# Performance work log

Hardware: AMD Instinct MI355X
Metric: run time of the kernel (lower is better)

Reference implementation:

```python
import jax, jax.numpy as jnp
import numpy as np

B, V, K = 4, 16384, 16
E, F, D, H, L, ITERS = 32, 2, 64, 4, 2, 10
NEG = -1e9


def setup_inputs() -> dict:
    key = jax.random.key(0)
    ks = jax.random.split(key, 24)
    def g(k, shape, fan_in):
        return jax.random.normal(k, shape, dtype=jnp.float32) * (fan_in ** -0.5)
    inp = {}
    inp["node_embeddings"] = jax.random.normal(ks[0], (B, V, E), dtype=jnp.float32)
    inp["node_features"] = jax.random.normal(ks[1], (B, V, F), dtype=jnp.float32)
    inp["demands"] = jax.random.normal(ks[2], (B, V, 1), dtype=jnp.float32)
    # padded adjacency list; value == V means masked (no neighbor)
    inp["adj_lst"] = jax.random.randint(ks[3], (B, V, K), 0, V + 1, dtype=jnp.int32)
    # precomputed inverse-adjacency indices; reference computes inflow by scatter-add instead
    inp["flow_indices"] = jax.random.randint(ks[4], (B, V, K), 0, V, dtype=jnp.int32)
    inp["num_nodes"] = V
    din = E + F
    inp["W_enc1"] = g(ks[5], (din, D), din); inp["b_enc1"] = jnp.zeros((D,), jnp.float32)
    inp["W_enc2"] = g(ks[6], (D, D), D); inp["b_enc2"] = jnp.zeros((D,), jnp.float32)
    inp["W_gat"] = g(ks[7], (H, D, D), D)
    inp["a_src"] = g(ks[8], (H, D), D)
    inp["a_dst"] = g(ks[9], (H, D), D)
    for i, nm in enumerate(["z", "r", "c"]):
        inp["W_" + nm] = g(ks[10 + 2 * i], (D, D), D)
        inp["U_" + nm] = g(ks[11 + 2 * i], (D, D), D)
        inp["b_" + nm] = jnp.zeros((D,), jnp.float32)
    inp["W_dec1"] = g(ks[16], (D, D), D); inp["b_dec1"] = jnp.zeros((D,), jnp.float32)
    inp["W_dec2"] = g(ks[17], (D, 1), D); inp["b_dec2"] = jnp.zeros((1,), jnp.float32)
    return inp


def _forward(node_embeddings, node_features, demands,
             W_enc1, b_enc1, W_enc2, b_enc2,
             W_gat, a_src, a_dst,
             W_z, U_z, b_z, W_r, U_r, b_r, W_c, U_c, b_c,
             W_dec1, b_dec1, W_dec2, b_dec2,
             adj_lst, num_nodes):
    Vn = num_nodes
    bidx = jnp.arange(adj_lst.shape[0])[:, None, None]  # [B,1,1]
    mask = adj_lst == Vn  # [B,V,K] padded slots

    # --- node encoder MLP (tanh, activate_final=True) ---
    x = jnp.concatenate([node_embeddings, node_features], axis=-1)
    h = jnp.tanh(x @ W_enc1 + b_enc1)
    h = jnp.tanh(h @ W_enc2 + b_enc2)

    def gather_nodes(t):
        # masked_gather: pad with a zero row so index == num_nodes reads zeros
        t_pad = jnp.concatenate([t, jnp.zeros_like(t[:, :1])], axis=1)  # [B,V+1,Dt]
        return t_pad[bidx, adj_lst]  # [B,V,K,Dt]

    # --- graph_layers x (AdjGAT + GRU) ---
    for _ in range(L):
        agg = 0.0
        for hd in range(H):
            t = h @ W_gat[hd]                       # [B,V,D]
            nb = gather_nodes(t)                    # [B,V,K,D]
            scores = (t @ a_src[hd])[:, :, None] + nb @ a_dst[hd]  # [B,V,K]
            attn = jax.nn.softmax(jnp.where(mask, NEG, scores), axis=-1)
            agg = agg + jnp.einsum('bvk,bvkd->bvd', attn, nb)
        m = jnp.tanh(agg / H)
        z = jax.nn.sigmoid(m @ W_z + h @ U_z + b_z)
        r = jax.nn.sigmoid(m @ W_r + h @ U_r + b_r)
        c = jnp.tanh(m @ W_c + (r * h) @ U_c + b_c)
        h = (1.0 - z) * h + z * c

    # --- decoder -> per-edge weights via masked gather + softmax ---
    node_w = jnp.tanh(h @ W_dec1 + b_dec1) @ W_dec2 + b_dec2   # [B,V,1]
    pw = gather_nodes(node_w)[..., 0]                          # [B,V,K]
    norm_w = jax.nn.softmax(jnp.where(mask, NEG, pw), axis=-1)

    # --- iterative min-cost-flow solver ---
    flow0 = norm_w * jax.nn.relu(-demands)  # sources (demand<0) push supply
    def body(carry, _):
        flow, _ = carry
        inflow = jnp.zeros((flow.shape[0], Vn + 1), flow.dtype)
        inflow = inflow.at[bidx, adj_lst].add(flow)[:, :Vn]    # [B,V]
        new = norm_w * jax.nn.relu(inflow[..., None] - demands)
        return (new, flow), None
    (flow, pflow), _ = jax.lax.scan(body, (flow0, flow0), None, length=ITERS)

    flow_cost = jnp.sum(flow * flow, axis=(1, 2))  # quadratic cost_fn
    return flow, flow_cost, norm_w, pflow


def reference(node_embeddings, node_features, demands, adj_lst, flow_indices, num_nodes,
              W_enc1, b_enc1, W_enc2, b_enc2, W_gat, a_src, a_dst,
              W_z, U_z, b_z, W_r, U_r, b_r, W_c, U_c, b_c,
              W_dec1, b_dec1, W_dec2, b_dec2):
    # flow_indices is the precomputed inverse adjacency; inflow is computed
    # equivalently here by scatter-add over adj_lst.
    return _forward(node_embeddings, node_features, demands,
                    W_enc1, b_enc1, W_enc2, b_enc2,
                    W_gat, a_src, a_dst,
                    W_z, U_z, b_z, W_r, U_r, b_r, W_c, U_c, b_c,
                    W_dec1, b_dec1, W_dec2, b_dec2,
                    adj_lst, num_nodes)
```

## Files before the change

### kernel.cpp

```cpp
#include <hip/hip_runtime.h>
#include <stdint.h>
#include <math.h>

#define BN 4
#define VN 16384
#define KN 16
#define HN 4
#define NN (BN*VN)
#define EN (VN*KN)
#define CAP 64
#define NEGC (-1.0e9f)

typedef __attribute__((ext_vector_type(8))) short short8;
typedef __attribute__((ext_vector_type(4))) float floatx4;
typedef __attribute__((ext_vector_type(2))) float floatx2;
typedef unsigned short u16;
typedef unsigned int u32;

#define OFF_H      0ull
#define OFF_M      8388608ull
#define OFF_T      16777216ull
#define OFF_SSRC   50331648ull
#define OFF_SDST   51380224ull
#define OFF_NW     52428800ull
#define OFF_NV     52690944ull
#define OFF_CNT    53215232ull
#define OFF_PG     53477376ull
#define OFF_PZR    (OFF_PG  + 32768ull)
#define OFF_PC     (OFF_PZR + 32768ull)
#define OFF_PE1    (OFF_PC  + 16384ull)
#define OFF_PE2    (OFF_PE1 + 8192ull)
#define OFF_PD1    (OFF_PE2 + 8192ull)

__device__ __forceinline__ u16 f2bf(float x){
  union { float f; unsigned int u; } c; c.f = x;
  unsigned int r = c.u + 0x7fffu + ((c.u >> 16) & 1u);
  return (u16)(r >> 16);
}
__device__ __forceinline__ float bf2f(u32 s){
  union { unsigned int u; float f; } c; c.u = s << 16;
  return c.f;
}
__device__ __forceinline__ float sigm(float x){ return 1.0f/(1.0f+expf(-x)); }

union S8 { short8 v; u16 u[8]; };

__global__ __launch_bounds__(256) void k_pack(
    const float* __restrict__ Wg,  const float* __restrict__ Wz, const float* __restrict__ Uz,
    const float* __restrict__ Wr,  const float* __restrict__ Ur, const float* __restrict__ Wc,
    const float* __restrict__ Uc,  const float* __restrict__ We1, const float* __restrict__ We2,
    const float* __restrict__ Wd1,
    u16* __restrict__ pg, u16* __restrict__ pzr, u16* __restrict__ pc,
    u16* __restrict__ pe1, u16* __restrict__ pe2, u16* __restrict__ pd1)
{
  int e = blockIdx.x*256 + threadIdx.x;
  int el; u16* dst; int CN; int region;
  if      (e < 16384){ el = e;        dst = pg;  CN = 2; region = 0; }
  else if (e < 32768){ el = e-16384;  dst = pzr; CN = 4; region = 1; }
  else if (e < 40960){ el = e-32768;  dst = pc;  CN = 4; region = 2; }
  else if (e < 45056){ el = e-40960;  dst = pe1; CN = 2; region = 3; }
  else if (e < 49152){ el = e-45056;  dst = pe2; CN = 2; region = 4; }
  else               { el = e-49152;  dst = pd1; CN = 2; region = 5; }
  int j    = el & 7;
  int lane = (el >> 3) & 63;
  int rest = el >> 9;
  int c  = rest % CN;
  int ng = rest / CN;
  int k  = c*32 + (lane>>4)*8 + j;
  int n  = ng*16 + (lane&15);
  float val = 0.0f;
  if (region == 0){
    val = Wg[(size_t)(n>>6)*4096 + k*64 + (n&63)];
  } else if (region == 1){
    int km = (k&3)*16 + ((k>>2)&15);
    if (n < 64) val = (k<64) ? Wz[km*64+n]      : Uz[(k-64)*64+n];
    else        val = (k<64) ? Wr[km*64+(n-64)] : Ur[(k-64)*64+(n-64)];
  } else if (region == 2){
    int km = (k&3)*16 + ((k>>2)&15);
    val = (k<64) ? Wc[km*64+n] : Uc[(k-64)*64+n];
  } else if (region == 3){
    val = (k<34) ? We1[k*64+n] : 0.0f;
  } else if (region == 4){
    val = We2[k*64+n];
  } else {
    val = Wd1[k*64+n];
  }
  dst[el] = f2bf(val);
}

template<int CN>
__device__ __forceinline__ void load_b(const u16* p, int chunk, int lane, short8 Bf[CN][4]){
  const short8* P = (const short8*)p;
  #pragma unroll
  for (int c=0;c<CN;c++)
    #pragma unroll
    for (int ng=0; ng<4; ng++)
      Bf[c][ng] = P[((chunk*4+ng)*CN + c)*64 + lane];
}

template<int CN>
__device__ __forceinline__ void mfma_tile(const short8* A, const short8 Bf[CN][4],
                                          floatx4 acc[4][4], int wave, int lane){
  #pragma unroll
  for (int c=0;c<CN;c++){
    #pragma unroll
    for (int mg=0;mg<4;mg++){
      short8 a = A[((wave*4+mg)*CN + c)*64 + lane];
      #pragma unroll
      for (int ng=0;ng<4;ng++)
        acc[mg][ng] = __builtin_amdgcn_mfma_f32_16x16x32_bf16(a, Bf[c][ng], acc[mg][ng], 0, 0, 0);
    }
  }
}

__device__ __forceinline__ void zero_acc(floatx4 acc[4][4]){
  #pragma unroll
  for (int mg=0;mg<4;mg++)
    #pragma unroll
    for (int ng=0;ng<4;ng++){
      floatx4 z = {0.f,0.f,0.f,0.f};
      acc[mg][ng] = z;
    }
}

__global__ __launch_bounds__(128) void k_enc(
    const float* __restrict__ emb, const float* __restrict__ feat,
    const u16* __restrict__ pe1, const u16* __restrict__ pe2,
    const float* __restrict__ be1, const float* __restrict__ be2,
    u16* __restrict__ hout, u32* __restrict__ cnt)
{
  cnt[blockIdx.x*128 + threadIdx.x] = 0u;
  __shared__ short8 A1[1024];
  __shared__ short8 A2[1024];
  const int tid = threadIdx.x;
  const int n0  = blockIdx.x * 128;
  for (int it=0; it<8; ++it){
    int slot = it*128 + tid;
    int row = slot >> 3, jc = slot & 7;
    S8 w;
    if (jc < 4){
      const float* s = emb + (size_t)(n0+row)*32 + jc*8;
      #pragma unroll
      for (int j=0;j<8;j++) w.u[j] = f2bf(s[j]);
    } else if (jc == 4){
      const float* s = feat + (size_t)(n0+row)*2;
      w.u[0] = f2bf(s[0]); w.u[1] = f2bf(s[1]);
      #pragma unroll
      for (int j=2;j<8;j++) w.u[j] = 0;
    } else {
      #pragma unroll
      for (int j=0;j<8;j++) w.u[j] = 0;
    }
    A1[((row>>4)*2 + (jc>>2))*64 + (jc&3)*16 + (row&15)] = w.v;
  }
  __syncthreads();
  const int wave = tid>>6, lane = tid&63, q = lane>>4, ml = lane&15;

  short8 Bf[2][4];
  load_b<2>(pe1, 0, lane, Bf);
  floatx4 acc[4][4];
  zero_acc(acc);
  mfma_tile<2>(A1, Bf, acc, wave, lane);

  u16* A2s = (u16*)A2;
  #pragma unroll
  for (int mg=0;mg<4;mg++){
    #pragma unroll
    for (int r=0;r<4;r++){
      int row_l = wave*64 + mg*16 + q*4 + r;
      #pragma unroll
      for (int ng=0;ng<4;ng++){
        int k2 = ng*16 + ml;
        float v = tanhf(acc[mg][ng][r] + be1[k2]);
        int c2 = k2>>5, q2=(k2>>3)&3, j2=k2&7;
        A2s[ (((row_l>>4)*2 + c2)*64 + q2*16 + (row_l&15))*8 + j2 ] = f2bf(v);
      }
    }
  }
  __syncthreads();

  load_b<2>(pe2, 0, lane, Bf);
  zero_acc(acc);
  mfma_tile<2>(A2, Bf, acc, wave, lane);
  #pragma unroll
  for (int mg=0;mg<4;mg++)
    #pragma unroll
    for (int r=0;r<4;r++){
      int row = n0 + wave*64 + mg*16 + q*4 + r;
      #pragma unroll
      for (int ng=0;ng<4;ng++){
        int col = ng*16 + ml;
        hout[(size_t)row*64 + col] = f2bf(tanhf(acc[mg][ng][r] + be2[col]));
      }
    }
}

__global__ __launch_bounds__(128) void k_t(
    const u16* __restrict__ h, const u16* __restrict__ pg,
    const float* __restrict__ asrc, const float* __restrict__ adst,
    u32* __restrict__ tq, float* __restrict__ ssrc, float* __restrict__ sdst)
{
  __shared__ short8 A[1024];
  const int tid = threadIdx.x;
  const int n0  = blockIdx.x * 128;
  const short8* hp = (const short8*)h;
  for (int it=0; it<8; ++it){
    int slot = it*128 + tid;
    int row = slot >> 3, jc = slot & 7;
    A[((row>>4)*2 + (jc>>2))*64 + (jc&3)*16 + (row&15)] = hp[(size_t)(n0+row)*8 + jc];
  }
  __syncthreads();
  const int wave = tid>>6, lane = tid&63, q = lane>>4, ml = lane&15;

  for (int chunk=0; chunk<4; ++chunk){
    short8 Bf[2][4];
    load_b<2>(pg, chunk, lane, Bf);
    floatx4 acc[4][4];
    zero_acc(acc);
    mfma_tile<2>(A, Bf, acc, wave, lane);

    float as[4], ad[4];
    #pragma unroll
    for (int ng=0;ng<4;ng++){
      as[ng] = asrc[chunk*64 + ng*16 + ml];
      ad[ng] = adst[chunk*64 + ng*16 + ml];
    }
    #pragma unroll
    for (int mg=0;mg<4;mg++){
      #pragma unroll
      for (int r=0;r<4;r++){
        int row = n0 + wave*64 + mg*16 + q*4 + r;
        float v0 = acc[mg][0][r], v1 = acc[mg][1][r];
        float v2 = acc[mg][2][r], v3 = acc[mg][3][r];
        int pk = __builtin_amdgcn_cvt_pk_fp8_f32(v0, v1, 0, false);
        pk     = __builtin_amdgcn_cvt_pk_fp8_f32(v2, v3, pk, true);
        tq[(size_t)row*64 + chunk*16 + ml] = (u32)pk;
        float ps = v0*as[0] + v1*as[1] + v2*as[2] + v3*as[3];
        float pd = v0*ad[0] + v1*ad[1] + v2*ad[2] + v3*ad[3];
        #pragma unroll
        for (int s=1;s<16;s<<=1){ ps += __shfl_xor(ps, s, 64); pd += __shfl_xor(pd, s, 64); }
        if (ml == 0){ ssrc[row*4 + chunk] = ps; sdst[row*4 + chunk] = pd; }
      }
    }
  }
}

__global__ __launch_bounds__(256) void k_attn(
    const int* __restrict__ adj, const u32* __restrict__ tq,
    const float* __restrict__ ssrc, const float* __restrict__ sdst,
    u16* __restrict__ m)
{
  const int wave = threadIdx.x>>6, lane = threadIdx.x&63;
  const int nid = blockIdx.x*4 + wave;
  const int b = nid >> 14;
  const int hd = lane>>4;
  int u = adj[(size_t)nid*16 + (lane&15)];
  float sc = (u == VN) ? NEGC : (ssrc[nid*4 + hd] + sdst[((size_t)b*VN + u)*4 + hd]);
  float mx = sc;
  #pragma unroll
  for (int s=1;s<16;s<<=1) mx = fmaxf(mx, __shfl_xor(mx, s, 64));
  float ex = expf(sc - mx);
  float sm = ex;
  #pragma unroll
  for (int s=1;s<16;s<<=1) sm += __shfl_xor(sm, s, 64);
  float attn = ex / sm;

  float a0=0.f, a1=0.f, a2=0.f, a3=0.f;
  const int srcl = lane & 48;
  #pragma unroll
  for (int k2=0;k2<16;k2++){
    int u2 = __shfl(u, k2, 64);
    float av = __shfl(attn, srcl + k2, 64);
    u32 w = tq[((size_t)b*VN + u2)*64 + lane];
    floatx2 f01 = __builtin_amdgcn_cvt_pk_f32_fp8((int)w, false);
    floatx2 f23 = __builtin_amdgcn_cvt_pk_f32_fp8((int)w, true);
    a0 += av*f01.x; a1 += av*f01.y; a2 += av*f23.x; a3 += av*f23.y;
  }
  a0 += __shfl_xor(a0,16,64); a0 += __shfl_xor(a0,32,64);
  a1 += __shfl_xor(a1,16,64); a1 += __shfl_xor(a1,32,64);
  a2 += __shfl_xor(a2,16,64); a2 += __shfl_xor(a2,32,64);
  a3 += __shfl_xor(a3,16,64); a3 += __shfl_xor(a3,32,64);
  if (lane < 16){
    union { uint2 v; u16 u[4]; } val;
    val.u[0] = f2bf(tanhf(a0*0.25f)); val.u[1] = f2bf(tanhf(a1*0.25f));
    val.u[2] = f2bf(tanhf(a2*0.25f)); val.u[3] = f2bf(tanhf(a3*0.25f));
    *(uint2*)(m + (size_t)nid*64 + lane*4) = val.v;
  }
}

__global__ __launch_bounds__(128) void k_gru(
    const u16* __restrict__ m, u16* __restrict__ h,
    const u16* __restrict__ pzr, const u16* __restrict__ pc_,
    const float* __restrict__ bz, const float* __restrict__ br,
    const float* __restrict__ bc_)
{
  __shared__ short8 A[2048];
  const int tid = threadIdx.x;
  const int n0  = blockIdx.x * 128;
  const short8* mp = (const short8*)m;
  const short8* hp = (const short8*)h;
  for (int it=0; it<16; ++it){
    int slot = it*128 + tid;
    int row = slot >> 4, jc = slot & 15;
    short8 w = (jc < 8) ? mp[(size_t)(n0+row)*8 + jc]
                        : hp[(size_t)(n0+row)*8 + (jc-8)];
    A[((row>>4)*4 + (jc>>2))*64 + (jc&3)*16 + (row&15)] = w;
  }
  __syncthreads();
  const int wave = tid>>6, lane = tid&63, q = lane>>4, ml = lane&15;

  short8 Bf[4][4];

  floatx4 zacc[4][4];
  load_b<4>(pzr, 0, lane, Bf);
  zero_acc(zacc);
  mfma_tile<4>(A, Bf, zacc, wave, lane);

  floatx4 acc[4][4];
  load_b<4>(pzr, 1, lane, Bf);
  zero_acc(acc);
  mfma_tile<4>(A, Bf, acc, wave, lane);

  floatx4 h_old[4][4];
  u16* As = (u16*)A;
  #pragma unroll
  for (int mg=0;mg<4;mg++){
    #pragma unroll
    for (int r=0;r<4;r++){
      int row_l = wave*64 + mg*16 + q*4 + r;
      int row   = n0 + row_l;
      #pragma unroll
      for (int ng=0;ng<4;ng++){
        int col = ng*16 + ml;
        float rv = sigm(acc[mg][ng][r] + br[col]);
        float hv = bf2f(h[(size_t)row*64 + col]);
        h_old[mg][ng][r] = hv;
        int kk = 64 + col;
        int c2 = kk>>5, q2 = (kk>>3)&3, j2 = kk&7;
        As[ (((row_l>>4)*4 + c2)*64 + q2*16 + (row_l&15))*8 + j2 ] = f2bf(hv*rv);
      }
    }
  }

  load_b<4>(pc_, 0, lane, Bf);
  zero_acc(acc);
  mfma_tile<4>(A, Bf, acc, wave, lane);

  #pragma unroll
  for (int mg=0;mg<4;mg++)
    #pragma unroll
    for (int r=0;r<4;r++){
      int row = n0 + wave*64 + mg*16 + q*4 + r;
      #pragma unroll
      for (int ng=0;ng<4;ng++){
        int col = ng*16 + ml;
        float zv = sigm(zacc[mg][ng][r] + bz[col]);
        float cv = tanhf(acc[mg][ng][r] + bc_[col]);
        float ho = h_old[mg][ng][r];
        h[(size_t)row*64 + col] = f2bf((1.f - zv)*ho + zv*cv);
      }
    }
}

__global__ __launch_bounds__(128) void k_dec(
    const u16* __restrict__ h, const u16* __restrict__ pd1,
    const float* __restrict__ bd1, const float* __restrict__ Wd2, const float* __restrict__ bd2,
    float* __restrict__ nodew, float* __restrict__ cost)
{
  {
    int t = blockIdx.x*128 + threadIdx.x;
    if (t < BN) cost[t] = 0.f;
  }
  __shared__ short8 A[1024];
  const int tid = threadIdx.x;
  const int n0  = blockIdx.x * 128;
  const short8* hp = (const short8*)h;
  for (int it=0; it<8; ++it){
    int slot = it*128 + tid;
    int row = slot >> 3, jc = slot & 7;
    A[((row>>4)*2 + (jc>>2))*64 + (jc&3)*16 + (row&15)] = hp[(size_t)(n0+row)*8 + jc];
  }
  __syncthreads();
  const int wave = tid>>6, lane = tid&63, q = lane>>4, ml = lane&15;

  short8 Bf[2][4];
  load_b<2>(pd1, 0, lane, Bf);
  floatx4 acc[4][4];
  zero_acc(acc);
  mfma_tile<2>(A, Bf, acc, wave, lane);

  float wd2l[4];
  #pragma unroll
  for (int ng=0;ng<4;ng++) wd2l[ng] = Wd2[ng*16 + ml];
  float b2 = bd2[0];
  #pragma unroll
  for (int mg=0;mg<4;mg++)
    #pragma unroll
    for (int r=0;r<4;r++){
      int row = n0 + wave*64 + mg*16 + q*4 + r;
      float ps = 0.f;
      #pragma unroll
      for (int ng=0;ng<4;ng++)
        ps += tanhf(acc[mg][ng][r] + bd1[ng*16+ml]) * wd2l[ng];
      #pragma unroll
      for (int s=1;s<16;s<<=1) ps += __shfl_xor(ps, s, 64);
      if (ml == 0) nodew[row] = ps + b2;
    }
}

__global__ __launch_bounds__(256) void k_pw(
    const int* __restrict__ adj, const float* __restrict__ nodew, const float* __restrict__ dem,
    float* __restrict__ normw, float* __restrict__ nv0,
    u32* __restrict__ cnt, u32* __restrict__ bucket)
{
  int e = blockIdx.x*256 + threadIdx.x;
  int node = e >> 4;
  int b = node >> 14;
  int u = adj[e];
  float pw = (u == VN) ? NEGC : nodew[(size_t)b*VN + u];
  float mx = pw;
  #pragma unroll
  for (int s=1;s<16;s<<=1) mx = fmaxf(mx, __shfl_xor(mx, s, 64));
  float ex = expf(pw - mx);
  float sm = ex;
  #pragma unroll
  for (int s=1;s<16;s<<=1) sm += __shfl_xor(sm, s, 64);
  float nw = ex / sm;
  normw[e] = nw;
  if ((e & 15) == 0) nv0[node] = fmaxf(-dem[node], 0.f);
  if (u < VN){
    int g = b*VN + u;
    u32 pos = atomicAdd(&cnt[g], 1u);
    if (pos < CAP)
      bucket[(size_t)g*CAP + pos] = ((u32)f2bf(nw) << 16) | (u32)(node & (VN-1));
  }
}

__global__ __launch_bounds__(256) void k_gather(
    const u32* __restrict__ cnt, const u32* __restrict__ bucket,
    const float* __restrict__ dem, const float* __restrict__ nvin, float* __restrict__ nvout)
{
  int tid = blockIdx.x*256 + threadIdx.x;
  int g = tid >> 4;
  int lane = tid & 15;
  int b = g >> 14;
  u32 n = cnt[g];
  if (n > CAP) n = CAP;
  const u32* bk = bucket + (size_t)g*CAP;
  const float* nb = nvin + (size_t)b*VN;
  float sum = 0.f;
  for (u32 i = (u32)lane; i < n; i += 16u){
    u32 r = bk[i];
    sum += bf2f(r >> 16) * nb[r & 0xFFFFu];
  }
  #pragma unroll
  for (int sh=1; sh<16; sh<<=1) sum += __shfl_xor(sum, sh, 64);
  if (lane == 0) nvout[g] = fmaxf(sum - dem[g], 0.f);
}

__global__ __launch_bounds__(256) void k_flows(
    const float* __restrict__ normw, const float* __restrict__ nv9,
    const float* __restrict__ nv10,
    float* __restrict__ pflow, float* __restrict__ flow, float* __restrict__ cost)
{
  int e = blockIdx.x*256 + threadIdx.x;
  int node = e >> 4;
  float w = normw[e];
  pflow[e] = w * nv9[node];
  float fl = w * nv10[node];
  flow[e] = fl;
  float ss = fl*fl;
  #pragma unroll
  for (int sh=1; sh<64; sh<<=1) ss += __shfl_xor(ss, sh, 64);
  __shared__ float part[4];
  if ((threadIdx.x & 63) == 0) part[threadIdx.x>>6] = ss;
  __syncthreads();
  if (threadIdx.x == 0) atomicAdd(cost + (e>>18), part[0]+part[1]+part[2]+part[3]);
}

extern "C" void kernel_launch(void* const* d_in, const int* in_sizes, int n_in,
                              void* d_out, int out_size, void* d_ws, size_t ws_size,
                              hipStream_t stream)
{
  const float* emb  = (const float*)d_in[0];
  const float* feat = (const float*)d_in[1];
  const float* dem  = (const float*)d_in[2];
  const int*   adj  = (const int*)  d_in[3];
  const float* We1 = (const float*)d_in[6];
  const float* be1 = (const float*)d_in[7];
  const float* We2 = (const float*)d_in[8];
  const float* be2 = (const float*)d_in[9];
  const float* Wg  = (const float*)d_in[10];
  const float* asrc= (const float*)d_in[11];
  const float* adst= (const float*)d_in[12];
  const float* Wz  = (const float*)d_in[13];
  const float* Uz  = (const float*)d_in[14];
  const float* bz  = (const float*)d_in[15];
  const float* Wr  = (const float*)d_in[16];
  const float* Ur  = (const float*)d_in[17];
  const float* br  = (const float*)d_in[18];
  const float* Wc  = (const float*)d_in[19];
  const float* Uc  = (const float*)d_in[20];
  const float* bc  = (const float*)d_in[21];
  const float* Wd1 = (const float*)d_in[22];
  const float* bd1 = (const float*)d_in[23];
  const float* Wd2 = (const float*)d_in[24];
  const float* bd2 = (const float*)d_in[25];

  char* ws = (char*)d_ws;
  u16*   h     = (u16*)  (ws + OFF_H);
  u16*   m     = (u16*)  (ws + OFF_M);
  u32*   tq    = (u32*)  (ws + OFF_T);
  u32*   bucket= (u32*)  (ws + OFF_T);
  float* ssrc  = (float*)(ws + OFF_SSRC);
  float* sdst  = (float*)(ws + OFF_SDST);
  float* nodew = (float*)(ws + OFF_NW);
  float* nv    = (float*)(ws + OFF_NV);
  u32*   cnt   = (u32*)  (ws + OFF_CNT);
  u16* pg  = (u16*)(ws + OFF_PG);
  u16* pzr = (u16*)(ws + OFF_PZR);
  u16* pc  = (u16*)(ws + OFF_PC);
  u16* pe1 = (u16*)(ws + OFF_PE1);
  u16* pe2 = (u16*)(ws + OFF_PE2);
  u16* pd1 = (u16*)(ws + OFF_PD1);
  float* nv0b = nv;
  float* nv1b = nv + NN;

  float* out0 = (float*)d_out;
  float* out1 = out0 + 1048576;
  float* out2 = out0 + 1048580;
  float* out3 = out0 + 2097156;

  k_pack<<<208, 256, 0, stream>>>(Wg, Wz, Uz, Wr, Ur, Wc, Uc, We1, We2, Wd1,
                                  pg, pzr, pc, pe1, pe2, pd1);
  k_enc<<<512, 128, 0, stream>>>(emb, feat, pe1, pe2, be1, be2, h, cnt);

  for (int l=0; l<2; ++l){
    k_t   <<<512, 128, 0, stream>>>(h, pg, asrc, adst, tq, ssrc, sdst);
    k_attn<<<16384, 256, 0, stream>>>(adj, tq, ssrc, sdst, m);
    k_gru <<<512, 128, 0, stream>>>(m, h, pzr, pc, bz, br, bc);
  }

  k_dec<<<512, 128, 0, stream>>>(h, pd1, bd1, Wd2, bd2, nodew, out1);
  k_pw <<<4096, 256, 0, stream>>>(adj, nodew, dem, out2, nv0b, cnt, bucket);

  for (int i=1; i<=10; ++i){
    float* in  = (i & 1) ? nv0b : nv1b;
    float* out = (i & 1) ? nv1b : nv0b;
    k_gather<<<4096, 256, 0, stream>>>(cnt, bucket, dem, in, out);
  }
  k_flows<<<4096, 256, 0, stream>>>(out2, nv1b, nv0b, out3, out0, out1);
}
```

Baseline: 481.3 us.

## Fold attention vectors into weights and build inverse adjacency with shared atomics

Precomputes W_gat·a_src and W_gat·a_dst per head during packing, so k_t gets the attention scores from one extra small MFMA on the bf16 hidden state. This replaces the per-row dot products and cross-lane shuffle reductions, and the src/dst scores are stored interleaved in one array. The scatter of edges into per-node buckets moves from global atomics in k_pw to a new k_build kernel. Each of its 64 blocks scans the full adjacency of one batch and counts only its 1024 targets with shared-memory atomics. This trades global atomic contention for 16x redundant reads of the adjacency and an extra launch, and computes the scores from bf16 inputs, which slightly changes precision.

```diff
diff --git a/kernel.cpp b/kernel.cpp
--- a/kernel.cpp
+++ b/kernel.cpp
@@ -20,8 +20,7 @@
 #define OFF_H      0ull
 #define OFF_M      8388608ull
 #define OFF_T      16777216ull
-#define OFF_SSRC   50331648ull
-#define OFF_SDST   51380224ull
+#define OFF_SS     50331648ull
 #define OFF_NW     52428800ull
 #define OFF_NV     52690944ull
 #define OFF_CNT    53215232ull
@@ -31,6 +30,7 @@
 #define OFF_PE1    (OFF_PC  + 16384ull)
 #define OFF_PE2    (OFF_PE1 + 8192ull)
 #define OFF_PD1    (OFF_PE2 + 8192ull)
+#define OFF_PAV    (OFF_PD1 + 8192ull)
 
 __device__ __forceinline__ u16 f2bf(float x){
   union { float f; unsigned int u; } c; c.f = x;
@@ -49,18 +49,21 @@
     const float* __restrict__ Wg,  const float* __restrict__ Wz, const float* __restrict__ Uz,
     const float* __restrict__ Wr,  const float* __restrict__ Ur, const float* __restrict__ Wc,
     const float* __restrict__ Uc,  const float* __restrict__ We1, const float* __restrict__ We2,
-    const float* __restrict__ Wd1,
+    const float* __restrict__ Wd1, const float* __restrict__ asrc, const float* __restrict__ adst,
     u16* __restrict__ pg, u16* __restrict__ pzr, u16* __restrict__ pc,
-    u16* __restrict__ pe1, u16* __restrict__ pe2, u16* __restrict__ pd1)
+    u16* __restrict__ pe1, u16* __restrict__ pe2, u16* __restrict__ pd1,
+    u16* __restrict__ pav)
 {
   int e = blockIdx.x*256 + threadIdx.x;
+  if (e >= 54272) return;
   int el; u16* dst; int CN; int region;
   if      (e < 16384){ el = e;        dst = pg;  CN = 2; region = 0; }
   else if (e < 32768){ el = e-16384;  dst = pzr; CN = 4; region = 1; }
   else if (e < 40960){ el = e-32768;  dst = pc;  CN = 4; region = 2; }
   else if (e < 45056){ el = e-40960;  dst = pe1; CN = 2; region = 3; }
   else if (e < 49152){ el = e-45056;  dst = pe2; CN = 2; region = 4; }
-  else               { el = e-49152;  dst = pd1; CN = 2; region = 5; }
+  else if (e < 53248){ el = e-49152;  dst = pd1; CN = 2; region = 5; }
+  else               { el = e-53248;  dst = pav; CN = 2; region = 6; }
   int j    = el & 7;
   int lane = (el >> 3) & 63;
   int rest = el >> 9;
@@ -82,8 +85,16 @@
     val = (k<34) ? We1[k*64+n] : 0.0f;
   } else if (region == 4){
     val = We2[k*64+n];
+  } else if (region == 5){
+    val = Wd1[k*64+n];
   } else {
-    val = Wd1[k*64+n];
+    int hd = (n>>1)&3, s = n&1;
+    const float* av = s ? (adst + hd*64) : (asrc + hd*64);
+    const float* wrow = Wg + (size_t)hd*4096 + k*64;
+    float acc = 0.f;
+    #pragma unroll 8
+    for (int d=0; d<64; d++) acc += wrow[d]*av[d];
+    val = acc;
   }
   dst[el] = f2bf(val);
 }
@@ -127,9 +138,8 @@
     const float* __restrict__ emb, const float* __restrict__ feat,
     const u16* __restrict__ pe1, const u16* __restrict__ pe2,
     const float* __restrict__ be1, const float* __restrict__ be2,
-    u16* __restrict__ hout, u32* __restrict__ cnt)
-{
-  cnt[blockIdx.x*128 + threadIdx.x] = 0u;
+    u16* __restrict__ hout)
+{
   __shared__ short8 A1[1024];
   __shared__ short8 A2[1024];
   const int tid = threadIdx.x;
@@ -196,9 +206,8 @@
 }
 
 __global__ __launch_bounds__(128) void k_t(
-    const u16* __restrict__ h, const u16* __restrict__ pg,
-    const float* __restrict__ asrc, const float* __restrict__ adst,
-    u32* __restrict__ tq, float* __restrict__ ssrc, float* __restrict__ sdst)
+    const u16* __restrict__ h, const u16* __restrict__ pg, const u16* __restrict__ pav,
+    u32* __restrict__ tq, float* __restrict__ ss)
 {
   __shared__ short8 A[1024];
   const int tid = threadIdx.x;
@@ -219,27 +228,32 @@
     zero_acc(acc);
     mfma_tile<2>(A, Bf, acc, wave, lane);
 
-    float as[4], ad[4];
-    #pragma unroll
-    for (int ng=0;ng<4;ng++){
-      as[ng] = asrc[chunk*64 + ng*16 + ml];
-      ad[ng] = adst[chunk*64 + ng*16 + ml];
-    }
     #pragma unroll
     for (int mg=0;mg<4;mg++){
       #pragma unroll
       for (int r=0;r<4;r++){
         int row = n0 + wave*64 + mg*16 + q*4 + r;
-        float v0 = acc[mg][0][r], v1 = acc[mg][1][r];
-        float v2 = acc[mg][2][r], v3 = acc[mg][3][r];
-        int pk = __builtin_amdgcn_cvt_pk_fp8_f32(v0, v1, 0, false);
-        pk     = __builtin_amdgcn_cvt_pk_fp8_f32(v2, v3, pk, true);
+        int pk = __builtin_amdgcn_cvt_pk_fp8_f32(acc[mg][0][r], acc[mg][1][r], 0, false);
+        pk     = __builtin_amdgcn_cvt_pk_fp8_f32(acc[mg][2][r], acc[mg][3][r], pk, true);
         tq[(size_t)row*64 + chunk*16 + ml] = (u32)pk;
-        float ps = v0*as[0] + v1*as[1] + v2*as[2] + v3*as[3];
-        float pd = v0*ad[0] + v1*ad[1] + v2*ad[2] + v3*ad[3];
-        #pragma unroll
-        for (int s=1;s<16;s<<=1){ ps += __shfl_xor(ps, s, 64); pd += __shfl_xor(pd, s, 64); }
-        if (ml == 0){ ssrc[row*4 + chunk] = ps; sdst[row*4 + chunk] = pd; }
+      }
+    }
+  }
+
+  const short8* Pv = (const short8*)pav;
+  short8 Bs0 = Pv[lane], Bs1 = Pv[64 + lane];
+  #pragma unroll
+  for (int mg=0;mg<4;mg++){
+    floatx4 sacc = {0.f,0.f,0.f,0.f};
+    short8 a0 = A[((wave*4+mg)*2 + 0)*64 + lane];
+    short8 a1 = A[((wave*4+mg)*2 + 1)*64 + lane];
+    sacc = __builtin_amdgcn_mfma_f32_16x16x32_bf16(a0, Bs0, sacc, 0, 0, 0);
+    sacc = __builtin_amdgcn_mfma_f32_16x16x32_bf16(a1, Bs1, sacc, 0, 0, 0);
+    if (ml < 8){
+      #pragma unroll
+      for (int r=0;r<4;r++){
+        int row = n0 + wave*64 + mg*16 + q*4 + r;
+        ss[(size_t)row*8 + ml] = sacc[r];
       }
     }
   }
@@ -247,15 +261,14 @@
 
 __global__ __launch_bounds__(256) void k_attn(
     const int* __restrict__ adj, const u32* __restrict__ tq,
-    const float* __restrict__ ssrc, const float* __restrict__ sdst,
-    u16* __restrict__ m)
+    const float* __restrict__ ss, u16* __restrict__ m)
 {
   const int wave = threadIdx.x>>6, lane = threadIdx.x&63;
   const int nid = blockIdx.x*4 + wave;
   const int b = nid >> 14;
   const int hd = lane>>4;
   int u = adj[(size_t)nid*16 + (lane&15)];
-  float sc = (u == VN) ? NEGC : (ssrc[nid*4 + hd] + sdst[((size_t)b*VN + u)*4 + hd]);
+  float sc = (u == VN) ? NEGC : (ss[(size_t)nid*8 + hd*2] + ss[((size_t)b*VN + u)*8 + hd*2 + 1]);
   float mx = sc;
   #pragma unroll
   for (int s=1;s<16;s<<=1) mx = fmaxf(mx, __shfl_xor(mx, s, 64));
@@ -410,8 +423,7 @@
 
 __global__ __launch_bounds__(256) void k_pw(
     const int* __restrict__ adj, const float* __restrict__ nodew, const float* __restrict__ dem,
-    float* __restrict__ normw, float* __restrict__ nv0,
-    u32* __restrict__ cnt, u32* __restrict__ bucket)
+    float* __restrict__ normw, float* __restrict__ nv0)
 {
   int e = blockIdx.x*256 + threadIdx.x;
   int node = e >> 4;
@@ -428,12 +440,31 @@
   float nw = ex / sm;
   normw[e] = nw;
   if ((e & 15) == 0) nv0[node] = fmaxf(-dem[node], 0.f);
-  if (u < VN){
-    int g = b*VN + u;
-    u32 pos = atomicAdd(&cnt[g], 1u);
-    if (pos < CAP)
-      bucket[(size_t)g*CAP + pos] = ((u32)f2bf(nw) << 16) | (u32)(node & (VN-1));
-  }
+}
+
+__global__ __launch_bounds__(1024) void k_build(
+    const int* __restrict__ adj, const float* __restrict__ normw,
+    u32* __restrict__ cnt, u32* __restrict__ bucket)
+{
+  __shared__ u32 cur[1024];
+  const int b  = blockIdx.x >> 4;
+  const int t0 = (blockIdx.x & 15) * 1024;
+  cur[threadIdx.x] = 0u;
+  __syncthreads();
+  const int*   a = adj   + (size_t)b*EN;
+  const float* w = normw + (size_t)b*EN;
+  for (int i = threadIdx.x; i < EN; i += 1024){
+    int t = a[i];
+    unsigned loc = (unsigned)(t - t0);
+    if (loc < 1024u){
+      u32 pos = atomicAdd(&cur[loc], 1u);
+      if (pos < CAP)
+        bucket[((size_t)(b*VN + t))*CAP + pos] = ((u32)f2bf(w[i]) << 16) | (u32)(i >> 4);
+    }
+  }
+  __syncthreads();
+  u32 c = cur[threadIdx.x];
+  cnt[b*VN + t0 + threadIdx.x] = (c < CAP) ? c : CAP;
 }
 
 __global__ __launch_bounds__(256) void k_gather(
@@ -445,7 +476,6 @@
   int lane = tid & 15;
   int b = g >> 14;
   u32 n = cnt[g];
-  if (n > CAP) n = CAP;
   const u32* bk = bucket + (size_t)g*CAP;
   const float* nb = nvin + (size_t)b*VN;
   float sum = 0.f;
@@ -512,8 +542,7 @@
   u16*   m     = (u16*)  (ws + OFF_M);
   u32*   tq    = (u32*)  (ws + OFF_T);
   u32*   bucket= (u32*)  (ws + OFF_T);
-  float* ssrc  = (float*)(ws + OFF_SSRC);
-  float* sdst  = (float*)(ws + OFF_SDST);
+  float* ss    = (float*)(ws + OFF_SS);
   float* nodew = (float*)(ws + OFF_NW);
   float* nv    = (float*)(ws + OFF_NV);
   u32*   cnt   = (u32*)  (ws + OFF_CNT);
@@ -523,6 +552,7 @@
   u16* pe1 = (u16*)(ws + OFF_PE1);
   u16* pe2 = (u16*)(ws + OFF_PE2);
   u16* pd1 = (u16*)(ws + OFF_PD1);
+  u16* pav = (u16*)(ws + OFF_PAV);
   float* nv0b = nv;
   float* nv1b = nv + NN;
 
@@ -531,18 +561,19 @@
   float* out2 = out0 + 1048580;
   float* out3 = out0 + 2097156;
 
-  k_pack<<<208, 256, 0, stream>>>(Wg, Wz, Uz, Wr, Ur, Wc, Uc, We1, We2, Wd1,
-                                  pg, pzr, pc, pe1, pe2, pd1);
-  k_enc<<<512, 128, 0, stream>>>(emb, feat, pe1, pe2, be1, be2, h, cnt);
+  k_pack<<<212, 256, 0, stream>>>(Wg, Wz, Uz, Wr, Ur, Wc, Uc, We1, We2, Wd1,
+                                  asrc, adst, pg, pzr, pc, pe1, pe2, pd1, pav);
+  k_enc<<<512, 128, 0, stream>>>(emb, feat, pe1, pe2, be1, be2, h);
 
   for (int l=0; l<2; ++l){
-    k_t   <<<512, 128, 0, stream>>>(h, pg, asrc, adst, tq, ssrc, sdst);
-    k_attn<<<16384, 256, 0, stream>>>(adj, tq, ssrc, sdst, m);
+    k_t   <<<512, 128, 0, stream>>>(h, pg, pav, tq, ss);
+    k_attn<<<16384, 256, 0, stream>>>(adj, tq, ss, m);
     k_gru <<<512, 128, 0, stream>>>(m, h, pzr, pc, bz, br, bc);
   }
 
   k_dec<<<512, 128, 0, stream>>>(h, pd1, bd1, Wd2, bd2, nodew, out1);
-  k_pw <<<4096, 256, 0, stream>>>(adj, nodew, dem, out2, nv0b, cnt, bucket);
+  k_pw <<<4096, 256, 0, stream>>>(adj, nodew, dem, out2, nv0b);
+  k_build<<<64, 1024, 0, stream>>>(adj, out2, cnt, bucket);
 
   for (int i=1; i<=10; ++i){
     float* in  = (i & 1) ? nv0b : nv1b;
```

After: 789.9 us. +64.1%, slower.
